# Kernel tuning notes

Measured on AMD Instinct MI355X. Metric: run time of the kernel, lower is better.

The kernel has to match this reference:

```python
import jax, jax.numpy as jnp
import numpy as np

ROUTING_ITERATIONS = 3
EPS = 1e-8


def squash(s):
    # standard CapsNet squash along the last (channels_per_unit) axis
    sq = jnp.sum(s * s, axis=-1, keepdims=True)
    return (sq / (1.0 + sq)) * s / jnp.sqrt(sq + EPS)


def setup_inputs() -> dict:
    key = jax.random.key(0)
    k1, k2 = jax.random.split(key)
    # inputs: (batch, input_channels, input_units)
    inputs = jax.random.normal(k1, (32, 8, 1152), dtype=jnp.float32)
    # weights: (input_units, num_units, input_channels, channels_per_unit)
    weights = jax.random.normal(k2, (1152, 10, 8, 16), dtype=jnp.float32)
    return {"inputs": inputs, "weights": weights}


def reference(inputs, weights):
    # (B, C, U) -> (B, U, C)
    votes = jnp.transpose(inputs, (0, 2, 1))
    # broadcast to (B, U, N, C, D): elementwise product as in the torch code
    pondered = weights[None, :, :, :, :] * votes[:, :, None, :, None]
    logits = jnp.zeros_like(pondered)
    out = pondered  # placeholder; overwritten in first iteration
    for _ in range(ROUTING_ITERATIONS):
        couplings = jax.nn.softmax(logits, axis=-1)
        out = squash(couplings * pondered)
        logits = logits + pondered * out  # agreement update
    # (B, U, N, C, D) -> (B, N, U, C, D)
    return jnp.transpose(out, (0, 2, 1, 3, 4))
```

## Files before the change

### kernel.cpp

```cpp
#include <hip/hip_runtime.h>

#define BB 32
#define UU 1152
#define NN 10
#define CC 8
#define DD 16
#define EPS 1e-8f
#define INV_LN2 1.44269504088896341f


typedef float f32x4 __attribute__((ext_vector_type(4)));

__device__ __forceinline__ float rcp_fast(float x) { return __builtin_amdgcn_rcpf(x); }
__device__ __forceinline__ float rsq_fast(float x) { return __builtin_amdgcn_rsqf(x); }

#if __has_builtin(__builtin_amdgcn_exp2f)
__device__ __forceinline__ float exp2_fast(float x) { return __builtin_amdgcn_exp2f(x); }
#else
__device__ __forceinline__ float exp2_fast(float x) { return __expf(x * 0.6931471805599453f); }
#endif

__device__ __forceinline__ float quad_sum(float x) {
    float y = __int_as_float(
        __builtin_amdgcn_update_dpp(0, __float_as_int(x), 0xB1, 0xF, 0xF, true));
    x += y;
    y = __int_as_float(
        __builtin_amdgcn_update_dpp(0, __float_as_int(x), 0x4E, 0xF, 0xF, true));
    return x + y;
}

__global__ __launch_bounds__(256, 8) void caps_route_kernel(
    const float* __restrict__ inputs,
    const float* __restrict__ weights,
    float* __restrict__ out)
{
    int t = blockIdx.x * blockDim.x + threadIdx.x;
    int sub = t & 3;
    int g   = t >> 2;
    int c   = g & 7;
    int g2  = g >> 3;
    int u   = g2 % UU;
    int b   = g2 / UU;

    float v = inputs[(b * CC + c) * UU + u];

    const float* wbase = weights + (u * NN * CC + c) * DD + sub * 4;
    float*       obase = out + ((b * NN * UU + u) * CC + c) * DD + sub * 4;

    #pragma unroll 2
    for (int n = 0; n < NN; ++n) {
        f32x4 w4 = *reinterpret_cast<const f32x4*>(wbase + n * (CC * DD));
        float p0 = w4.x * v, p1 = w4.y * v, p2 = w4.z * v, p3 = w4.w * v;
        float q0 = p0 * p0, q1 = p1 * p1, q2 = p2 * p2, q3 = p3 * p3;

        float sq0 = quad_sum((q0 + q1) + (q2 + q3)) * (1.0f / 256.0f);
        float kk = sq0 * rcp_fast(1.0f + sq0) * rsq_fast(sq0 + EPS)
                   * (INV_LN2 / 16.0f);
        float L0 = kk * q0, L1 = kk * q1, L2 = kk * q2, L3 = kk * q3;

        {
            float e0 = exp2_fast(L0), e1 = exp2_fast(L1);
            float e2 = exp2_fast(L2), e3 = exp2_fast(L3);
            float S  = quad_sum((e0 + e1) + (e2 + e3));
            float m0 = e0 * q0, m1 = e1 * q1, m2 = e2 * q2, m3 = e3 * q3;
            float A  = quad_sum((m0 * e0 + m1 * e1) + (m2 * e2 + m3 * e3));
            float Ssq = S * S;
            float k = A * rsq_fast(fmaf(EPS, Ssq, A)) * rcp_fast(Ssq + A)
                      * INV_LN2;
            L0 = fmaf(k, m0, L0); L1 = fmaf(k, m1, L1);
            L2 = fmaf(k, m2, L2); L3 = fmaf(k, m3, L3);
        }

        {
            float e0 = exp2_fast(L0), e1 = exp2_fast(L1);
            float e2 = exp2_fast(L2), e3 = exp2_fast(L3);
            float S  = quad_sum((e0 + e1) + (e2 + e3));
            float t0 = e0 * p0, t1 = e1 * p1, t2 = e2 * p2, t3 = e3 * p3;
            float A  = quad_sum((t0 * t0 + t1 * t1) + (t2 * t2 + t3 * t3));
            float Ssq = S * S;
            float ko = A * rsq_fast(fmaf(EPS, Ssq, A)) * rcp_fast(Ssq + A);
            f32x4 r;
            r.x = ko * t0; r.y = ko * t1; r.z = ko * t2; r.w = ko * t3;
            *reinterpret_cast<f32x4*>(obase + n * (UU * CC * DD)) = r;
        }
    }
}

extern "C" void kernel_launch(void* const* d_in, const int* in_sizes, int n_in,
                              void* d_out, int out_size, void* d_ws, size_t ws_size,
                              hipStream_t stream) {
    const float* inputs  = (const float*)d_in[0];
    const float* weights = (const float*)d_in[1];
    float* out = (float*)d_out;

    const long long total = (long long)BB * UU * CC * 4;
    const int block = 256;
    const int grid = (int)(total / block);
    caps_route_kernel<<<grid, block, 0, stream>>>(inputs, weights, out);
}
```

Baseline: 43.33 us.

## Use 8 elements per thread, batch-major block order, and prefetch weights

Each thread now handles 8 of the 16 D elements, so a reduction needs one DPP exchange instead of two and the thread count is halved. Blocks are ordered so that 32 consecutive blocks share the same 16 units across all batches, improving L2 reuse of weights. Weight loads are software-prefetched two iterations ahead in a non-unrolled loop. The cost is more registers per thread and half as many threads, which may lower occupancy and latency hiding.

```diff
diff --git a/kernel.cpp b/kernel.cpp
--- a/kernel.cpp
+++ b/kernel.cpp
@@ -20,68 +20,86 @@
 __device__ __forceinline__ float exp2_fast(float x) { return __expf(x * 0.6931471805599453f); }
 #endif
 
-__device__ __forceinline__ float quad_sum(float x) {
+__device__ __forceinline__ float pair_sum(float x) {
     float y = __int_as_float(
         __builtin_amdgcn_update_dpp(0, __float_as_int(x), 0xB1, 0xF, 0xF, true));
-    x += y;
-    y = __int_as_float(
-        __builtin_amdgcn_update_dpp(0, __float_as_int(x), 0x4E, 0xF, 0xF, true));
     return x + y;
 }
 
-__global__ __launch_bounds__(256, 8) void caps_route_kernel(
+__device__ __forceinline__ float hsum4(f32x4 a) {
+    return (a.x + a.y) + (a.z + a.w);
+}
+
+__device__ __forceinline__ f32x4 exp2_v4(f32x4 a) {
+    f32x4 r;
+    r.x = exp2_fast(a.x); r.y = exp2_fast(a.y);
+    r.z = exp2_fast(a.z); r.w = exp2_fast(a.w);
+    return r;
+}
+
+__global__ __launch_bounds__(256) void caps_route_kernel(
     const float* __restrict__ inputs,
     const float* __restrict__ weights,
     float* __restrict__ out)
 {
-    int t = blockIdx.x * blockDim.x + threadIdx.x;
-    int sub = t & 3;
-    int g   = t >> 2;
-    int c   = g & 7;
-    int g2  = g >> 3;
-    int u   = g2 % UU;
-    int b   = g2 / UU;
+    int tid = threadIdx.x;
+    int bi  = blockIdx.x;
+    int b   = bi & 31;
+    int ub  = bi >> 5;
+
+    int sub    = tid & 1;
+    int c      = (tid >> 1) & 7;
+    int ulocal = tid >> 4;
+    int u      = ub * 16 + ulocal;
 
     float v = inputs[(b * CC + c) * UU + u];
 
-    const float* wbase = weights + (u * NN * CC + c) * DD + sub * 4;
-    float*       obase = out + ((b * NN * UU + u) * CC + c) * DD + sub * 4;
+    const float* wbase = weights + (u * NN * CC + c) * DD + sub * 8;
+    float*       obase = out + ((b * NN * UU + u) * CC + c) * DD + sub * 8;
+    const int WSTRIDE = CC * DD;
+    const int OSTRIDE = UU * CC * DD;
 
-    #pragma unroll 2
+    f32x4 wa0 = *reinterpret_cast<const f32x4*>(wbase);
+    f32x4 wb0 = *reinterpret_cast<const f32x4*>(wbase + 4);
+    f32x4 wa1 = *reinterpret_cast<const f32x4*>(wbase + WSTRIDE);
+    f32x4 wb1 = *reinterpret_cast<const f32x4*>(wbase + WSTRIDE + 4);
+
+    #pragma unroll 1
     for (int n = 0; n < NN; ++n) {
-        f32x4 w4 = *reinterpret_cast<const f32x4*>(wbase + n * (CC * DD));
-        float p0 = w4.x * v, p1 = w4.y * v, p2 = w4.z * v, p3 = w4.w * v;
-        float q0 = p0 * p0, q1 = p1 * p1, q2 = p2 * p2, q3 = p3 * p3;
+        f32x4 wa = wa0, wb = wb0;
+        wa0 = wa1; wb0 = wb1;
+        int np = (n + 2 < NN) ? (n + 2) : (NN - 1);
+        wa1 = *reinterpret_cast<const f32x4*>(wbase + np * WSTRIDE);
+        wb1 = *reinterpret_cast<const f32x4*>(wbase + np * WSTRIDE + 4);
 
-        float sq0 = quad_sum((q0 + q1) + (q2 + q3)) * (1.0f / 256.0f);
+        f32x4 pa = wa * v, pb = wb * v;
+        f32x4 qa = pa * pa, qb = pb * pb;
+
+        float sq0 = pair_sum(hsum4(qa + qb)) * (1.0f / 256.0f);
         float kk = sq0 * rcp_fast(1.0f + sq0) * rsq_fast(sq0 + EPS)
                    * (INV_LN2 / 16.0f);
-        float L0 = kk * q0, L1 = kk * q1, L2 = kk * q2, L3 = kk * q3;
+        f32x4 La = kk * qa, Lb = kk * qb;
 
         {
-            float e0 = exp2_fast(L0), e1 = exp2_fast(L1);
-            float e2 = exp2_fast(L2), e3 = exp2_fast(L3);
-            float S  = quad_sum((e0 + e1) + (e2 + e3));
-            float m0 = e0 * q0, m1 = e1 * q1, m2 = e2 * q2, m3 = e3 * q3;
-            float A  = quad_sum((m0 * e0 + m1 * e1) + (m2 * e2 + m3 * e3));
+            f32x4 ea = exp2_v4(La), eb = exp2_v4(Lb);
+            float S = pair_sum(hsum4(ea + eb));
+            f32x4 ma = ea * qa, mb = eb * qb;
+            float A = pair_sum(hsum4(ma * ea + mb * eb));
             float Ssq = S * S;
             float k = A * rsq_fast(fmaf(EPS, Ssq, A)) * rcp_fast(Ssq + A)
                       * INV_LN2;
-            L0 = fmaf(k, m0, L0); L1 = fmaf(k, m1, L1);
-            L2 = fmaf(k, m2, L2); L3 = fmaf(k, m3, L3);
+            La += k * ma;  Lb += k * mb;
         }
 
         {
-            float e0 = exp2_fast(L0), e1 = exp2_fast(L1);
-            float e2 = exp2_fast(L2), e3 = exp2_fast(L3);
-            float S  = quad_sum((e0 + e1) + (e2 + e3));
-            float t0 = e0 * p0, t1 = e1 * p1, t2 = e2 * p2, t3 = e3 * p3;
-            float A  = quad_sum((t0 * t0 + t1 * t1) + (t2 * t2 + t3 * t3));
+            f32x4 ea = exp2_v4(La), eb = exp2_v4(Lb);
+            float S = pair_sum(hsum4(ea + eb));
+            f32x4 ta = ea * pa, tb = eb * pb;
+            float A = pair_sum(hsum4(ta * ta + tb * tb));
             float Ssq = S * S;
             float ko = A * rsq_fast(fmaf(EPS, Ssq, A)) * rcp_fast(Ssq + A);
-            f32x4 r;
-            r.x = ko * t0; r.y = ko * t1; r.z = ko * t2; r.w = ko * t3;
-            *reinterpret_cast<f32x4*>(obase + n * (UU * CC * DD)) = r;
+            *reinterpret_cast<f32x4*>(obase + n * OSTRIDE)     = ko * ta;
+            *reinterpret_cast<f32x4*>(obase + n * OSTRIDE + 4) = ko * tb;
         }
     }
 }
@@ -93,7 +111,7 @@
     const float* weights = (const float*)d_in[1];
     float* out = (float*)d_out;
 
-    const long long total = (long long)BB * UU * CC * 4;
+    const long long total = (long long)BB * UU * CC * 2;
     const int block = 256;
     const int grid = (int)(total / block);
     caps_route_kernel<<<grid, block, 0, stream>>>(inputs, weights, out);
```

Result: no change. 43.52 us (+0.5%).
